# Performance work log

Measured on AMD Instinct MI355X. Metric: run time of the kernel, lower is better.

Reference implementation:

```python
import jax, jax.numpy as jnp
import numpy as np
from jax.scipy.special import gammaln

B, N, F, K = 128, 29, 64, 64
MAXZ, NITER, NPATH = 56, 2, 20
CUTOFF = 5.0


def setup_inputs() -> dict:
    key = jax.random.key(0)
    ks = jax.random.split(key, 16)
    atomic_numbers = jax.random.randint(ks[0], (B, N), 1, MAXZ)
    positions = jax.random.normal(ks[1], (B, N, 3), dtype=jnp.float32) * 2.0
    Ef = jax.random.normal(ks[2], (B, 3), dtype=jnp.float32)
    # fully connected molecular graph (all ordered pairs i != j), E = N*(N-1) = 812
    ii, jj = np.meshgrid(np.arange(N), np.arange(N), indexing="ij")
    m = ii != jj
    dst_idx = jnp.asarray(ii[m], dtype=jnp.int32)
    src_idx = jnp.asarray(jj[m], dtype=jnp.int32)
    s = 1.0 / np.sqrt(F)
    t = 0.2  # tensor-product path weight scale (keeps activations bounded)
    return {
        "atomic_numbers": atomic_numbers, "positions": positions, "Ef": Ef,
        "dst_idx": dst_idx, "src_idx": src_idx,
        "embed": jax.random.normal(ks[3], (MAXZ, F), dtype=jnp.float32) * s,
        "mp_basis_w": jax.random.normal(ks[4], (NITER, K, F), dtype=jnp.float32) / np.sqrt(K),
        "mp_tp_w": jax.random.normal(ks[5], (NITER, NPATH, F), dtype=jnp.float32) * t,
        "d1_w": jax.random.normal(ks[6], (NITER, 2, 2, F, F), dtype=jnp.float32) * s,
        "d1_b": jnp.zeros((NITER, 2, F), dtype=jnp.float32),
        "d2_w": jax.random.normal(ks[7], (NITER, 2, 2, F, F), dtype=jnp.float32) * s,
        "d2_b": jnp.zeros((NITER, 2, F), dtype=jnp.float32),
        "tens_w": jax.random.normal(ks[8], (NITER, NPATH, F), dtype=jnp.float32) * t,
        "td_dense_w": jax.random.normal(ks[9], (NITER, 2, 2, F, F), dtype=jnp.float32) * s,
        "td_tp_w": jax.random.normal(ks[10], (NITER, NPATH, F), dtype=jnp.float32) * t,
        "out_w": jax.random.normal(ks[11], (F,), dtype=jnp.float32) * s,
        "element_bias": jax.random.normal(ks[12], (MAXZ,), dtype=jnp.float32) * 0.1,
    }


def _tp(a, b, w):
    """Channelwise Clebsch-Gordan tensor product for max_degree=1 with parity channels.
    a, b: (M, 2, 4, F) with axis1 = (regular, pseudo), axis2 = (l=0, l=1 x/y/z).
    w: (20, F) learned per-path weights (5 l-paths x 4 parity combos)."""
    M, Fd = a.shape[0], a.shape[-1]
    sr = jnp.zeros((M, Fd), a.dtype); sp = jnp.zeros((M, Fd), a.dtype)
    vr = jnp.zeros((M, 3, Fd), a.dtype); vp = jnp.zeros((M, 3, Fd), a.dtype)
    idx = 0
    for p1 in range(2):
        for p2 in range(2):
            s1 = a[:, p1, 0]; v1 = a[:, p1, 1:4]
            s2 = b[:, p2, 0]; v2 = b[:, p2, 1:4]
            pl0a = 1 - 2 * p1; pl0b = 1 - 2 * p2   # parity of l=0 slot
            pl1a = -(1 - 2 * p1); pl1b = -(1 - 2 * p2)  # parity of l=1 slot
            tt = w[idx] * s1 * s2
            if pl0a * pl0b == 1: sr = sr + tt
            else: sp = sp + tt
            tt = w[idx + 1] * s1[:, None, :] * v2
            if pl0a * pl1b == -1: vr = vr + tt
            else: vp = vp + tt
            tt = w[idx + 2] * v1 * s2[:, None, :]
            if pl1a * pl0b == -1: vr = vr + tt
            else: vp = vp + tt
            tt = w[idx + 3] * jnp.sum(v1 * v2, axis=1)
            if pl1a * pl1b == 1: sr = sr + tt
            else: sp = sp + tt
            tt = w[idx + 4] * jnp.cross(v1, v2, axis=1)
            if pl1a * pl1b == -1: vr = vr + tt
            else: vp = vp + tt
            idx += 5
    reg = jnp.concatenate([sr[:, None, :], vr], axis=1)
    pse = jnp.concatenate([sp[:, None, :], vp], axis=1)
    return jnp.stack([reg, pse], axis=1)  # (M, 2, 4, F)


def _dense(x, W, b=None):
    # per-(parity, degree) linear map over features; W: (2, 2, F, F), b: (2, F)
    s = jnp.einsum("npf,pfg->npg", x[:, :, 0, :], W[:, 0])
    v = jnp.einsum("npdf,pfg->npdg", x[:, :, 1:4, :], W[:, 1])
    if b is not None:
        s = s + b
    return jnp.concatenate([s[:, :, None, :], v], axis=2)


def _silu(x):
    # gated equivariant silu: silu on scalars, sigmoid(scalar) gate on vectors
    s = x[:, :, 0:1, :]
    g = jax.nn.sigmoid(s)
    return jnp.concatenate([s * g, x[:, :, 1:4, :] * g], axis=2)


def _radial(r):
    # reciprocal Bernstein radial basis with smooth cutoff
    k = jnp.arange(K, dtype=r.dtype)
    logc = gammaln(float(K)) - gammaln(k + 1.0) - gammaln(float(K) - k)
    u = 1.0 / (1.0 + r)
    logb = logc + k * jnp.log(u)[:, None] + (K - 1.0 - k) * jnp.log(jnp.maximum(1.0 - u, 1e-12))[:, None]
    x2 = (r / CUTOFF) ** 2
    fcut = jnp.where(x2 < 1.0, jnp.exp(1.0 - 1.0 / jnp.maximum(1.0 - x2, 1e-12)), 0.0)
    return jnp.exp(logb) * fcut[:, None]  # (E, K)


def reference(atomic_numbers, positions, Ef, dst_idx, src_idx, embed, mp_basis_w,
              mp_tp_w, d1_w, d1_b, d2_w, d2_b, tens_w, td_dense_w, td_tp_w,
              out_w, element_bias):
    Bsz, Nn = atomic_numbers.shape
    BN = Bsz * Nn
    Fd = embed.shape[-1]
    pos = positions.reshape(-1, 3)
    Z = atomic_numbers.reshape(-1)
    offsets = (jnp.arange(Bsz, dtype=dst_idx.dtype) * Nn)
    dstf = (dst_idx[None, :] + offsets[:, None]).reshape(-1)  # (B*E,)
    srcf = (src_idx[None, :] + offsets[:, None]).reshape(-1)
    disp = pos[srcf] - pos[dstf]                               # (B*E, 3)
    r = jnp.sqrt(jnp.sum(disp * disp, axis=-1) + 1e-12)
    unit = disp / r[:, None]
    sph = jnp.concatenate([jnp.ones_like(r)[:, None], unit], axis=-1)  # (B*E, 4)
    basis = sph[:, :, None] * _radial(r)[:, None, :]           # (B*E, 4, K)

    x = jnp.zeros((BN, 2, 4, Fd), dtype=positions.dtype)
    x = x.at[:, 0, 0, :].set(embed[Z])

    xEFv = jnp.concatenate([jnp.ones((Bsz, 1), positions.dtype), Ef], axis=-1)  # (B, 4)
    xEF = jnp.repeat(xEFv, Nn, axis=0)                          # (BN, 4)
    xEF = jnp.broadcast_to(xEF[:, None, :, None], (BN, 2, 4, Fd))

    for i in range(NITER):
        bproj = jnp.einsum("edk,kf->edf", basis, mp_basis_w[i])  # (B*E, 4, F)
        bfeat = jnp.stack([bproj, jnp.zeros_like(bproj)], axis=1)  # (B*E, 2, 4, F)
        msg = _tp(x[srcf], bfeat, mp_tp_w[i])
        if i == NITER - 1:  # last iteration: max_degree=0 messages
            msg = msg * jnp.array([1.0, 0.0, 0.0, 0.0], msg.dtype)[None, None, :, None]
        y = jax.ops.segment_sum(msg, dstf, num_segments=BN)
        x = x + y
        h = _dense(x, d1_w[i], d1_b[i])
        h = _silu(h)
        h = _dense(h, d2_w[i], d2_b[i])
        x = h + y
        x = x + _tp(x, xEF, tens_w[i])          # Tensor()(x, xEF)
        x = _tp(x, _dense(x, td_dense_w[i]), td_tp_w[i])  # TensorDense

    s = x[:, 0, 0, :]  # degree-0 regular channel
    atomic_energies = s @ out_w + element_bias[Z]
    energy = atomic_energies.reshape(Bsz, Nn).sum(axis=1)
    return energy
```

## Files before the change

kernel.cpp:

```cpp
#include <hip/hip_runtime.h>

#define NB 128
#define NA 29
#define BN (NB*NA)
#define FD 64


template<bool LAST>
__global__ __launch_bounds__(256) void fmsg_kernel(
    const int*   __restrict__ Z,
    const float* __restrict__ pos,
    const float* __restrict__ src,
    const float* __restrict__ wtp,
    const float* __restrict__ Wb,
    float* __restrict__ y,
    float* __restrict__ out)
{
  __shared__ float elu[28], el1mu[28], efc[28];
  __shared__ float us[28][3];
  __shared__ float rads[28][FD];
  __shared__ float emb_sh[NA][FD];
  __shared__ float yred[4][4][FD];
  const int bn = blockIdx.x, b = bn / NA, n = bn - b*NA;
  const int tid = threadIdx.x, lane = tid & 63, wv = tid >> 6;

  if constexpr (!LAST) {
    if (bn < NB && tid == 0) out[bn] = 0.0f;
  }

  if (tid < 28) {
    const int jr = tid, j = jr + (jr >= n ? 1 : 0);
    const float dx = pos[(b*NA+j)*3+0] - pos[(b*NA+n)*3+0];
    const float dy = pos[(b*NA+j)*3+1] - pos[(b*NA+n)*3+1];
    const float dz = pos[(b*NA+j)*3+2] - pos[(b*NA+n)*3+2];
    const float r  = sqrtf(dx*dx + dy*dy + dz*dz + 1e-12f);
    const float ri = 1.0f / r;
    us[jr][0] = dx*ri; us[jr][1] = dy*ri; us[jr][2] = dz*ri;
    const float u  = 1.0f/(1.0f + r);
    elu[jr]   = logf(u);
    el1mu[jr] = logf(fmaxf(1.0f - u, 1e-12f));
    const float x2 = (r*0.2f)*(r*0.2f);
    efc[jr] = (x2 < 1.0f) ? expf(1.0f - 1.0f/fmaxf(1.0f - x2, 1e-12f)) : 0.0f;
  }
  if constexpr (!LAST) {
    for (int idx = tid; idx < NA*FD; idx += 256)
      emb_sh[idx>>6][idx&63] = src[Z[b*NA + (idx>>6)]*FD + (idx&63)];
  }
  const float kk   = (float)lane;
  const float logc = lgammaf(64.0f) - lgammaf(kk + 1.0f) - lgammaf(64.0f - kk);
  __syncthreads();

  #pragma unroll
  for (int i = 0; i < 7; ++i) {
    const int e = wv*7 + i;
    rads[e][lane] = expf(logc + kk*elu[e] + (63.0f - kk)*el1mu[e]) * efc[e];
  }
  float wb[64];
  #pragma unroll
  for (int k = 0; k < 64; ++k) wb[k] = Wb[k*FD + lane];

  float y0 = 0.0f, y1 = 0.0f, y2 = 0.0f, y3 = 0.0f, y4 = 0.0f;
  const float wm0 = wtp[0*FD + lane];
  const float wm1 = LAST ? 0.0f : wtp[1*FD + lane];
  const float wm3 = LAST ? wtp[3*FD + lane]  : 0.0f;
  const float wm5 = LAST ? wtp[10*FD + lane] : 0.0f;
  const float wm8 = LAST ? wtp[13*FD + lane] : 0.0f;

  #pragma unroll
  for (int i = 0; i < 7; ++i) {
    const int jr = wv*7 + i;
    float a0 = 0.0f;
    #pragma unroll
    for (int k4 = 0; k4 < 16; ++k4) {
      const float4 rv = *(const float4*)&rads[jr][k4*4];
      a0 += wb[k4*4+0]*rv.x + wb[k4*4+1]*rv.y + wb[k4*4+2]*rv.z + wb[k4*4+3]*rv.w;
    }
    const int j = jr + (jr >= n ? 1 : 0);
    const float ux = us[jr][0], uy = us[jr][1], uz = us[jr][2];
    if constexpr (!LAST) {
      const float t0 = a0 * emb_sh[j][lane];
      y0 += wm0*t0;
      const float t1 = wm1*t0;
      y1 += t1*ux; y2 += t1*uy; y3 += t1*uz;
    } else {
      const float* xj = src + (size_t)(b*NA + j)*512 + lane;
      const float s1   = xj[0];
      const float dot1 = xj[64]*ux + xj[128]*uy + xj[192]*uz;
      const float s1p  = xj[256];
      const float dotp = xj[320]*ux + xj[384]*uy + xj[448]*uz;
      y0 += a0*(wm0*s1  + wm3*dot1);
      y4 += a0*(wm5*s1p + wm8*dotp);
    }
  }

  if constexpr (!LAST) {
    yred[wv][0][lane] = y0; yred[wv][1][lane] = y1;
    yred[wv][2][lane] = y2; yred[wv][3][lane] = y3;
  } else {
    yred[wv][0][lane] = y0; yred[wv][1][lane] = y4;
  }
  __syncthreads();
  if (wv == 0) {
    if constexpr (!LAST) {
      #pragma unroll
      for (int c = 0; c < 4; ++c) {
        const float s = yred[0][c][lane] + yred[1][c][lane]
                      + yred[2][c][lane] + yred[3][c][lane];
        y[(size_t)bn*256 + c*64 + lane] = s;
      }
    } else {
      const float s0 = yred[0][0][lane] + yred[1][0][lane]
                     + yred[2][0][lane] + yred[3][0][lane];
      const float s4 = yred[0][1][lane] + yred[1][1][lane]
                     + yred[2][1][lane] + yred[3][1][lane];
      y[(size_t)bn*512 + lane]       = s0;
      y[(size_t)bn*512 + 256 + lane] = s4;
    }
  }
}

__device__ __forceinline__ void tp20(const float* a, const float* bb,
                                     const float* w, float* o)
{
  #pragma unroll
  for (int p1 = 0; p1 < 2; ++p1) {
    #pragma unroll
    for (int p2 = 0; p2 < 2; ++p2) {
      const float* w5 = w + 5*(2*p1 + p2);
      const float s1 = a[p1*4+0], x1 = a[p1*4+1], y1 = a[p1*4+2], z1 = a[p1*4+3];
      const float s2 = bb[p2*4+0], x2 = bb[p2*4+1], y2 = bb[p2*4+2], z2 = bb[p2*4+3];
      const int so = (p1 == p2) ? 0 : 4;
      const int vo = 4 - so;
      o[so+0] += w5[0]*(s1*s2) + w5[3]*(x1*x2 + y1*y2 + z1*z2);
      o[so+1] += w5[1]*(s1*x2) + w5[2]*(x1*s2);
      o[so+2] += w5[1]*(s1*y2) + w5[2]*(y1*s2);
      o[so+3] += w5[1]*(s1*z2) + w5[2]*(z1*s2);
      o[vo+1] += w5[4]*(y1*z2 - z1*y2);
      o[vo+2] += w5[4]*(z1*x2 - x1*z2);
      o[vo+3] += w5[4]*(x1*y2 - y1*x2);
    }
  }
}

__device__ __forceinline__ void stage2(float* __restrict__ wst,
                                       const float* __restrict__ src, int tid)
{
  const float4* s = (const float4*)src;
  float4* d = (float4*)wst;
  #pragma unroll
  for (int i = 0; i < 8; ++i) d[tid + i*256] = s[tid + i*256];
}

__device__ __forceinline__ void denseP2(const float* __restrict__ wst,
                                        const float* __restrict__ rA,
                                        const float* __restrict__ rB,
                                        float bs, int g,
                                        float oA[4], float oB[4])
{
  float a0A = bs, a0B = bs;
  #pragma unroll
  for (int f4 = 0; f4 < 16; ++f4) {
    const float w0 = wst[(f4*4+0)*64+g], w1 = wst[(f4*4+1)*64+g];
    const float w2 = wst[(f4*4+2)*64+g], w3 = wst[(f4*4+3)*64+g];
    const float4 xA = *(const float4*)&rA[f4*4];
    const float4 xB = *(const float4*)&rB[f4*4];
    a0A += w0*xA.x + w1*xA.y + w2*xA.z + w3*xA.w;
    a0B += w0*xB.x + w1*xB.y + w2*xB.z + w3*xB.w;
  }
  oA[0] = a0A; oB[0] = a0B;
  float a1A = 0, a2A = 0, a3A = 0, a1B = 0, a2B = 0, a3B = 0;
  #pragma unroll
  for (int f4 = 0; f4 < 16; ++f4) {
    const float w0 = wst[4096+(f4*4+0)*64+g], w1 = wst[4096+(f4*4+1)*64+g];
    const float w2 = wst[4096+(f4*4+2)*64+g], w3 = wst[4096+(f4*4+3)*64+g];
    const float4 aA = *(const float4*)&rA[ 64+f4*4];
    const float4 bA = *(const float4*)&rA[128+f4*4];
    const float4 cA = *(const float4*)&rA[192+f4*4];
    const float4 aB = *(const float4*)&rB[ 64+f4*4];
    const float4 bB = *(const float4*)&rB[128+f4*4];
    const float4 cB = *(const float4*)&rB[192+f4*4];
    a1A += w0*aA.x + w1*aA.y + w2*aA.z + w3*aA.w;
    a2A += w0*bA.x + w1*bA.y + w2*bA.z + w3*bA.w;
    a3A += w0*cA.x + w1*cA.y + w2*cA.z + w3*cA.w;
    a1B += w0*aB.x + w1*aB.y + w2*aB.z + w3*aB.w;
    a2B += w0*bB.x + w1*bB.y + w2*bB.z + w3*bB.w;
    a3B += w0*cB.x + w1*cB.y + w2*cB.z + w3*cB.w;
  }
  oA[1] = a1A; oA[2] = a2A; oA[3] = a3A;
  oB[1] = a1B; oB[2] = a2B; oB[3] = a3B;
}

template<bool LAST>
__global__ __launch_bounds__(256) void node_kernel(
    const int*   __restrict__ Z,
    const float* __restrict__ embed,
    const float* __restrict__ Ef,
    const float* __restrict__ d1w, const float* __restrict__ d1b,
    const float* __restrict__ d2w, const float* __restrict__ d2b,
    const float* __restrict__ tens_w,
    const float* __restrict__ tdw,
    const float* __restrict__ td_tp_w,
    const float* __restrict__ out_w,
    const float* __restrict__ ebias,
    const float* __restrict__ xin,
    const float* __restrict__ yin,
    float* __restrict__ xout,
    float* __restrict__ out)
{
  __shared__ float wst[2*64*64];
  __shared__ float row[8][8][FD];
  __shared__ float c4_sh[FD];
  const int tid = threadIdx.x, r = tid >> 6, g = tid & 63;
  const int ndA = blockIdx.x*8 + r*2, ndB = ndA + 1;
  float* rowA = &row[r*2+0][0][0];
  float* rowB = &row[r*2+1][0][0];

  if constexpr (!LAST) {
    if (tid < 64) { const float v = d1b[64+tid]; wst[tid] = v/(1.0f + expf(-v)); }
    __syncthreads();
    if (tid < 64) {
      float acc = d2b[64 + tid];
      for (int f = 0; f < 64; ++f) acc += d2w[8192 + f*64 + tid] * wst[f];
      c4_sh[tid] = acc;
    }
    __syncthreads();
  }

  float yA[4], yB[4];
  float y0A = 0, y4A = 0, y0B = 0, y4B = 0;
  if constexpr (!LAST) {
    #pragma unroll
    for (int c = 0; c < 4; ++c) {
      yA[c] = yin[(size_t)ndA*256 + c*64 + g];
      yB[c] = yin[(size_t)ndB*256 + c*64 + g];
    }
    rowA[g] = embed[Z[ndA]*FD + g] + yA[0];
    rowB[g] = embed[Z[ndB]*FD + g] + yB[0];
    #pragma unroll
    for (int c = 1; c < 4; ++c) { rowA[c*64+g] = yA[c]; rowB[c*64+g] = yB[c]; }
  } else {
    y0A = yin[(size_t)ndA*512 + g];     y4A = yin[(size_t)ndA*512 + 256 + g];
    y0B = yin[(size_t)ndB*512 + g];     y4B = yin[(size_t)ndB*512 + 256 + g];
    #pragma unroll
    for (int pc = 0; pc < 8; ++pc) {
      float vA = xin[(size_t)ndA*512 + pc*64 + g];
      float vB = xin[(size_t)ndB*512 + pc*64 + g];
      if (pc == 0) { vA += y0A; vB += y0B; }
      if (pc == 4) { vA += y4A; vB += y4B; }
      rowA[pc*64+g] = vA; rowB[pc*64+g] = vB;
    }
  }
  stage2(wst, d1w, tid);
  __syncthreads();

  {
    float hA[4], hB[4];
    denseP2(wst, rowA, rowB, d1b[g], g, hA, hB);
    const float sA = 1.0f/(1.0f + expf(-hA[0]));
    const float sB = 1.0f/(1.0f + expf(-hB[0]));
    rowA[g] = hA[0]*sA; rowB[g] = hB[0]*sB;
    #pragma unroll
    for (int c = 1; c < 4; ++c) { rowA[c*64+g] = hA[c]*sA; rowB[c*64+g] = hB[c]*sB; }
  }
  __syncthreads();
  if constexpr (LAST) {
    stage2(wst, d1w + 8192, tid);
    __syncthreads();
    float hA[4], hB[4];
    denseP2(wst, rowA + 256, rowB + 256, d1b[64+g], g, hA, hB);
    const float sA = 1.0f/(1.0f + expf(-hA[0]));
    const float sB = 1.0f/(1.0f + expf(-hB[0]));
    rowA[256+g] = hA[0]*sA; rowB[256+g] = hB[0]*sB;
    #pragma unroll
    for (int c = 1; c < 4; ++c) { rowA[256+c*64+g] = hA[c]*sA; rowB[256+c*64+g] = hB[c]*sB; }
    __syncthreads();
  }
  stage2(wst, d2w, tid);
  __syncthreads();

  float x2A[8], x2B[8];
  {
    float oA[4], oB[4];
    denseP2(wst, rowA, rowB, d2b[g], g, oA, oB);
    #pragma unroll
    for (int c = 0; c < 4; ++c) { x2A[c] = oA[c]; x2B[c] = oB[c]; }
  }
  if constexpr (!LAST) {
    #pragma unroll
    for (int c = 0; c < 4; ++c) { x2A[c] += yA[c]; x2B[c] += yB[c]; }
    const float c4v = c4_sh[g];
    x2A[4] = c4v; x2B[4] = c4v;
    x2A[5] = x2A[6] = x2A[7] = 0.0f;
    x2B[5] = x2B[6] = x2B[7] = 0.0f;
  } else {
    x2A[0] += y0A; x2B[0] += y0B;
    __syncthreads();
    stage2(wst, d2w + 8192, tid);
    __syncthreads();
    float oA[4], oB[4];
    denseP2(wst, rowA + 256, rowB + 256, d2b[64+g], g, oA, oB);
    x2A[4] = oA[0] + y4A; x2A[5] = oA[1]; x2A[6] = oA[2]; x2A[7] = oA[3];
    x2B[4] = oB[0] + y4B; x2B[5] = oB[1]; x2B[6] = oB[2]; x2B[7] = oB[3];
  }

  float x3A[8], x3B[8];
  {
    float w20[20];
    #pragma unroll
    for (int q = 0; q < 20; ++q) w20[q] = tens_w[q*FD + g];
    const int bA = ndA / NA, bB = ndB / NA;
    {
      const float bbv[8] = {1.0f, Ef[bA*3+0], Ef[bA*3+1], Ef[bA*3+2],
                            1.0f, Ef[bA*3+0], Ef[bA*3+1], Ef[bA*3+2]};
      float o[8] = {0,0,0,0,0,0,0,0};
      tp20(x2A, bbv, w20, o);
      #pragma unroll
      for (int pc = 0; pc < 8; ++pc) { x3A[pc] = x2A[pc] + o[pc]; rowA[pc*64+g] = x3A[pc]; }
    }
    {
      const float bbv[8] = {1.0f, Ef[bB*3+0], Ef[bB*3+1], Ef[bB*3+2],
                            1.0f, Ef[bB*3+0], Ef[bB*3+1], Ef[bB*3+2]};
      float o[8] = {0,0,0,0,0,0,0,0};
      tp20(x2B, bbv, w20, o);
      #pragma unroll
      for (int pc = 0; pc < 8; ++pc) { x3B[pc] = x2B[pc] + o[pc]; rowB[pc*64+g] = x3B[pc]; }
    }
  }
  __syncthreads();
  stage2(wst, tdw, tid);
  __syncthreads();

  float tdA[8], tdB[8];
  {
    float oA[4], oB[4];
    denseP2(wst, rowA, rowB, 0.0f, g, oA, oB);
    #pragma unroll
    for (int c = 0; c < 4; ++c) { tdA[c] = oA[c]; tdB[c] = oB[c]; }
  }
  __syncthreads();
  stage2(wst, tdw + 8192, tid);
  __syncthreads();
  {
    float oA[4], oB[4];
    denseP2(wst, rowA + 256, rowB + 256, 0.0f, g, oA, oB);
    #pragma unroll
    for (int c = 0; c < 4; ++c) { tdA[4+c] = oA[c]; tdB[4+c] = oB[c]; }
  }

  if constexpr (LAST) {
    const float wa = td_tp_w[0*FD+g],  wb = td_tp_w[3*FD+g];
    const float wc = td_tp_w[15*FD+g], wd = td_tp_w[18*FD+g];
    const float ow = out_w[g];
    float pA = ow * (wa*(x3A[0]*tdA[0])
                   + wb*(x3A[1]*tdA[1] + x3A[2]*tdA[2] + x3A[3]*tdA[3])
                   + wc*(x3A[4]*tdA[4])
                   + wd*(x3A[5]*tdA[5] + x3A[6]*tdA[6] + x3A[7]*tdA[7]));
    float pB = ow * (wa*(x3B[0]*tdB[0])
                   + wb*(x3B[1]*tdB[1] + x3B[2]*tdB[2] + x3B[3]*tdB[3])
                   + wc*(x3B[4]*tdB[4])
                   + wd*(x3B[5]*tdB[5] + x3B[6]*tdB[6] + x3B[7]*tdB[7]));
    #pragma unroll
    for (int off = 32; off > 0; off >>= 1) {
      pA += __shfl_xor(pA, off, 64);
      pB += __shfl_xor(pB, off, 64);
    }
    if (g == 0) {
      atomicAdd(&out[ndA/NA], pA + ebias[Z[ndA]]);
      atomicAdd(&out[ndB/NA], pB + ebias[Z[ndB]]);
    }
  } else {
    float w20[20];
    #pragma unroll
    for (int q = 0; q < 20; ++q) w20[q] = td_tp_w[q*FD + g];
    {
      float o[8] = {0,0,0,0,0,0,0,0};
      tp20(x3A, tdA, w20, o);
      #pragma unroll
      for (int pc = 0; pc < 8; ++pc) xout[(size_t)ndA*512 + pc*64 + g] = o[pc];
    }
    {
      float o[8] = {0,0,0,0,0,0,0,0};
      tp20(x3B, tdB, w20, o);
      #pragma unroll
      for (int pc = 0; pc < 8; ++pc) xout[(size_t)ndB*512 + pc*64 + g] = o[pc];
    }
  }
}

extern "C" void kernel_launch(void* const* d_in, const int* in_sizes, int n_in,
                              void* d_out, int out_size, void* d_ws, size_t ws_size,
                              hipStream_t stream)
{
  (void)in_sizes; (void)n_in; (void)out_size; (void)ws_size;
  const int*   Z     = (const int*)  d_in[0];
  const float* pos   = (const float*)d_in[1];
  const float* Ef    = (const float*)d_in[2];
  const float* embed = (const float*)d_in[5];
  const float* mpbw  = (const float*)d_in[6];
  const float* mptpw = (const float*)d_in[7];
  const float* d1w   = (const float*)d_in[8];
  const float* d1b   = (const float*)d_in[9];
  const float* d2w   = (const float*)d_in[10];
  const float* d2b   = (const float*)d_in[11];
  const float* tensw = (const float*)d_in[12];
  const float* tdw   = (const float*)d_in[13];
  const float* tdtpw = (const float*)d_in[14];
  const float* outw  = (const float*)d_in[15];
  const float* ebias = (const float*)d_in[16];
  float* out = (float*)d_out;

  float* xg = (float*)d_ws;
  float* yg = xg + (size_t)BN*512;

  fmsg_kernel<false><<<BN, 256, 0, stream>>>(Z, pos, embed, mptpw, mpbw, yg, out);
  node_kernel<false><<<BN/8, 256, 0, stream>>>(Z, embed, Ef,
      d1w, d1b, d2w, d2b, tensw, tdw, tdtpw, outw, ebias,
      nullptr, yg, xg, nullptr);
  fmsg_kernel<true><<<BN, 256, 0, stream>>>(Z, pos, xg, mptpw + 1280,
      mpbw + 4096, yg, nullptr);
  node_kernel<true><<<BN/8, 256, 0, stream>>>(Z, embed, Ef,
      d1w + 16384, d1b + 128, d2w + 16384, d2b + 128, tensw + 1280,
      tdw + 16384, tdtpw + 1280, outw, ebias,
      xg, yg, nullptr, out);
}
```

Before: 122.7 us.

## Double-buffer dense weight staging with register prefetch in node kernel

Splits weight staging into a global-to-register load and a register-to-shared write. The next weight matrix is prefetched into registers while the current dense layer computes, and two shared buffers alternate so one barrier per stage replaces two. The c4 constant is now computed by every thread into a register instead of by 64 threads into shared memory, which removes one barrier. In exchange the kernel holds 32 extra registers for the prefetch, and the extra shared buffer may lower occupancy.

```diff
diff --git a/kernel.cpp b/kernel.cpp
--- a/kernel.cpp
+++ b/kernel.cpp
@@ -142,13 +142,19 @@
   }
 }
 
-__device__ __forceinline__ void stage2(float* __restrict__ wst,
-                                       const float* __restrict__ src, int tid)
+__device__ __forceinline__ void stageLoad(float4 L[8],
+                                          const float* __restrict__ src, int tid)
 {
   const float4* s = (const float4*)src;
+  #pragma unroll
+  for (int i = 0; i < 8; ++i) L[i] = s[tid + i*256];
+}
+__device__ __forceinline__ void stageWrite(float* __restrict__ wst,
+                                           const float4 L[8], int tid)
+{
   float4* d = (float4*)wst;
   #pragma unroll
-  for (int i = 0; i < 8; ++i) d[tid + i*256] = s[tid + i*256];
+  for (int i = 0; i < 8; ++i) d[tid + i*256] = L[i];
 }
 
 __device__ __forceinline__ void denseP2(const float* __restrict__ wst,
@@ -207,24 +213,27 @@
     float* __restrict__ xout,
     float* __restrict__ out)
 {
-  __shared__ float wst[2*64*64];
-  __shared__ float row[8][8][FD];
-  __shared__ float c4_sh[FD];
+  __shared__ float wstA[8192];
+  __shared__ float wstB[8192];
+  __shared__ float rows[8][512];
   const int tid = threadIdx.x, r = tid >> 6, g = tid & 63;
   const int ndA = blockIdx.x*8 + r*2, ndB = ndA + 1;
-  float* rowA = &row[r*2+0][0][0];
-  float* rowB = &row[r*2+1][0][0];
-
-  if constexpr (!LAST) {
-    if (tid < 64) { const float v = d1b[64+tid]; wst[tid] = v/(1.0f + expf(-v)); }
-    __syncthreads();
-    if (tid < 64) {
-      float acc = d2b[64 + tid];
-      for (int f = 0; f < 64; ++f) acc += d2w[8192 + f*64 + tid] * wst[f];
-      c4_sh[tid] = acc;
-    }
-    __syncthreads();
-  }
+  float* rowA = rows[r*2+0];
+  float* rowB = rows[r*2+1];
+  float4 L[8];
+
+  float c4r = 0.0f;
+  if constexpr (!LAST) {
+    if (tid < 64) { const float v = d1b[64+tid]; rows[0][tid] = v/(1.0f + expf(-v)); }
+    __syncthreads();
+    float acc = d2b[64 + g];
+    #pragma unroll 8
+    for (int f = 0; f < 64; ++f) acc += d2w[8192 + f*64 + g] * rows[0][f];
+    c4r = acc;
+    __syncthreads();
+  }
+
+  stageLoad(L, d1w, tid);
 
   float yA[4], yB[4];
   float y0A = 0, y4A = 0, y0B = 0, y4B = 0;
@@ -250,61 +259,84 @@
       rowA[pc*64+g] = vA; rowB[pc*64+g] = vB;
     }
   }
-  stage2(wst, d1w, tid);
+  stageWrite(wstA, L, tid);
+  stageLoad(L, LAST ? d1w + 8192 : d2w, tid);
   __syncthreads();
 
   {
     float hA[4], hB[4];
-    denseP2(wst, rowA, rowB, d1b[g], g, hA, hB);
+    denseP2(wstA, rowA, rowB, d1b[g], g, hA, hB);
     const float sA = 1.0f/(1.0f + expf(-hA[0]));
     const float sB = 1.0f/(1.0f + expf(-hB[0]));
     rowA[g] = hA[0]*sA; rowB[g] = hB[0]*sB;
     #pragma unroll
     for (int c = 1; c < 4; ++c) { rowA[c*64+g] = hA[c]*sA; rowB[c*64+g] = hB[c]*sB; }
   }
+  stageWrite(wstB, L, tid);
+  stageLoad(L, LAST ? d2w : tdw, tid);
   __syncthreads();
+
   if constexpr (LAST) {
-    stage2(wst, d1w + 8192, tid);
-    __syncthreads();
     float hA[4], hB[4];
-    denseP2(wst, rowA + 256, rowB + 256, d1b[64+g], g, hA, hB);
+    denseP2(wstB, rowA + 256, rowB + 256, d1b[64+g], g, hA, hB);
     const float sA = 1.0f/(1.0f + expf(-hA[0]));
     const float sB = 1.0f/(1.0f + expf(-hB[0]));
     rowA[256+g] = hA[0]*sA; rowB[256+g] = hB[0]*sB;
     #pragma unroll
     for (int c = 1; c < 4; ++c) { rowA[256+c*64+g] = hA[c]*sA; rowB[256+c*64+g] = hB[c]*sB; }
-    __syncthreads();
-  }
-  stage2(wst, d2w, tid);
-  __syncthreads();
+    stageWrite(wstA, L, tid);
+    stageLoad(L, d2w + 8192, tid);
+    __syncthreads();
+  }
 
   float x2A[8], x2B[8];
   {
     float oA[4], oB[4];
-    denseP2(wst, rowA, rowB, d2b[g], g, oA, oB);
+    denseP2(LAST ? wstA : wstB, rowA, rowB, d2b[g], g, oA, oB);
     #pragma unroll
     for (int c = 0; c < 4; ++c) { x2A[c] = oA[c]; x2B[c] = oB[c]; }
   }
+  float x3A[8], x3B[8];
   if constexpr (!LAST) {
     #pragma unroll
     for (int c = 0; c < 4; ++c) { x2A[c] += yA[c]; x2B[c] += yB[c]; }
-    const float c4v = c4_sh[g];
-    x2A[4] = c4v; x2B[4] = c4v;
+    x2A[4] = c4r; x2B[4] = c4r;
     x2A[5] = x2A[6] = x2A[7] = 0.0f;
     x2B[5] = x2B[6] = x2B[7] = 0.0f;
+    float w20[20];
+    #pragma unroll
+    for (int q = 0; q < 20; ++q) w20[q] = tens_w[q*FD + g];
+    const int bA = ndA / NA, bB = ndB / NA;
+    {
+      const float bbv[8] = {1.0f, Ef[bA*3+0], Ef[bA*3+1], Ef[bA*3+2],
+                            1.0f, Ef[bA*3+0], Ef[bA*3+1], Ef[bA*3+2]};
+      float o[8] = {0,0,0,0,0,0,0,0};
+      tp20(x2A, bbv, w20, o);
+      #pragma unroll
+      for (int pc = 0; pc < 8; ++pc) { x3A[pc] = x2A[pc] + o[pc]; rowA[pc*64+g] = x3A[pc]; }
+    }
+    {
+      const float bbv[8] = {1.0f, Ef[bB*3+0], Ef[bB*3+1], Ef[bB*3+2],
+                            1.0f, Ef[bB*3+0], Ef[bB*3+1], Ef[bB*3+2]};
+      float o[8] = {0,0,0,0,0,0,0,0};
+      tp20(x2B, bbv, w20, o);
+      #pragma unroll
+      for (int pc = 0; pc < 8; ++pc) { x3B[pc] = x2B[pc] + o[pc]; rowB[pc*64+g] = x3B[pc]; }
+    }
+    stageWrite(wstA, L, tid);
+    stageLoad(L, tdw + 8192, tid);
+    __syncthreads();
   } else {
     x2A[0] += y0A; x2B[0] += y0B;
-    __syncthreads();
-    stage2(wst, d2w + 8192, tid);
-    __syncthreads();
-    float oA[4], oB[4];
-    denseP2(wst, rowA + 256, rowB + 256, d2b[64+g], g, oA, oB);
-    x2A[4] = oA[0] + y4A; x2A[5] = oA[1]; x2A[6] = oA[2]; x2A[7] = oA[3];
-    x2B[4] = oB[0] + y4B; x2B[5] = oB[1]; x2B[6] = oB[2]; x2B[7] = oB[3];
-  }
-
-  float x3A[8], x3B[8];
-  {
+    stageWrite(wstB, L, tid);
+    stageLoad(L, tdw, tid);
+    __syncthreads();
+    {
+      float oA[4], oB[4];
+      denseP2(wstB, rowA + 256, rowB + 256, d2b[64+g], g, oA, oB);
+      x2A[4] = oA[0] + y4A; x2A[5] = oA[1]; x2A[6] = oA[2]; x2A[7] = oA[3];
+      x2B[4] = oB[0] + y4B; x2B[5] = oB[1]; x2B[6] = oB[2]; x2B[7] = oB[3];
+    }
     float w20[20];
     #pragma unroll
     for (int q = 0; q < 20; ++q) w20[q] = tens_w[q*FD + g];
@@ -325,24 +357,23 @@
       #pragma unroll
       for (int pc = 0; pc < 8; ++pc) { x3B[pc] = x2B[pc] + o[pc]; rowB[pc*64+g] = x3B[pc]; }
     }
-  }
-  __syncthreads();
-  stage2(wst, tdw, tid);
-  __syncthreads();
+    stageWrite(wstA, L, tid);
+    stageLoad(L, tdw + 8192, tid);
+    __syncthreads();
+  }
 
   float tdA[8], tdB[8];
   {
     float oA[4], oB[4];
-    denseP2(wst, rowA, rowB, 0.0f, g, oA, oB);
+    denseP2(wstA, rowA, rowB, 0.0f, g, oA, oB);
     #pragma unroll
     for (int c = 0; c < 4; ++c) { tdA[c] = oA[c]; tdB[c] = oB[c]; }
   }
-  __syncthreads();
-  stage2(wst, tdw + 8192, tid);
+  stageWrite(wstB, L, tid);
   __syncthreads();
   {
     float oA[4], oB[4];
-    denseP2(wst, rowA + 256, rowB + 256, 0.0f, g, oA, oB);
+    denseP2(wstB, rowA + 256, rowB + 256, 0.0f, g, oA, oB);
     #pragma unroll
     for (int c = 0; c < 4; ++c) { tdA[4+c] = oA[c]; tdB[4+c] = oB[c]; }
   }
```

After: 177.7 us. +44.9%, slower.

## Keep node activations in registers and broadcast via readlane in node dense layers

Applied to the files above, without the earlier changes.

Node-kernel dense layers now keep per-node activations in registers and broadcast each input feature across the wavefront with readlane, instead of staging rows in shared memory. Weights are staged transposed with an XOR swizzle so each lane reads float4 rows of its own output column without bank conflicts. This removes the shared row buffer, the c4 shared buffer and several barriers. The cost is 64 scalar readlanes per input vector per layer plus a more scattered shared-memory store pattern during weight staging.

```diff
diff --git a/kernel.cpp b/kernel.cpp
--- a/kernel.cpp
+++ b/kernel.cpp
@@ -142,49 +142,68 @@
   }
 }
 
-__device__ __forceinline__ void stage2(float* __restrict__ wst,
-                                       const float* __restrict__ src, int tid)
+__device__ __forceinline__ float rl(float v, int l)
+{
+  return __uint_as_float((unsigned)__builtin_amdgcn_readlane((int)__float_as_uint(v), l));
+}
+
+__device__ __forceinline__ void stage2s(float* __restrict__ wst,
+                                        const float* __restrict__ src, int tid)
 {
   const float4* s = (const float4*)src;
   float4* d = (float4*)wst;
   #pragma unroll
-  for (int i = 0; i < 8; ++i) d[tid + i*256] = s[tid + i*256];
-}
-
-__device__ __forceinline__ void denseP2(const float* __restrict__ wst,
-                                        const float* __restrict__ rA,
-                                        const float* __restrict__ rB,
-                                        float bs, int g,
-                                        float oA[4], float oB[4])
-{
+  for (int i = 0; i < 8; ++i) {
+    const int idx = tid + i*256;
+    const int sel = idx >> 10, rem = idx & 1023;
+    const int gg = rem >> 4, f4 = rem & 15;
+    const float4 v = s[idx];
+    const int fline = gg;
+    const int f = rem >> 4;
+    const int g4 = rem & 15;
+    #pragma unroll
+    for (int q = 0; q < 4; ++q) {
+      const int g = g4*4 + q;
+      const int fq = f >> 2, fj = f & 3;
+      ((float*)&d[(sel*64 + g)*16 + (fq ^ (g & 7))])[fj] = (&v.x)[q];
+    }
+    (void)fline;
+  }
+}
+
+__device__ __forceinline__ void denseRL2(
+    const float* __restrict__ wst, int g,
+    float sA, float v1A, float v2A, float v3A,
+    float sB, float v1B, float v2B, float v3B,
+    float bs, float oA[4], float oB[4])
+{
+  const int swb = g & 7;
+  const float4* w0 = (const float4*)wst + g*16;
+  const float4* w1 = (const float4*)wst + (64+g)*16;
   float a0A = bs, a0B = bs;
   #pragma unroll
   for (int f4 = 0; f4 < 16; ++f4) {
-    const float w0 = wst[(f4*4+0)*64+g], w1 = wst[(f4*4+1)*64+g];
-    const float w2 = wst[(f4*4+2)*64+g], w3 = wst[(f4*4+3)*64+g];
-    const float4 xA = *(const float4*)&rA[f4*4];
-    const float4 xB = *(const float4*)&rB[f4*4];
-    a0A += w0*xA.x + w1*xA.y + w2*xA.z + w3*xA.w;
-    a0B += w0*xB.x + w1*xB.y + w2*xB.z + w3*xB.w;
+    const float4 w = w0[f4 ^ swb];
+    #pragma unroll
+    for (int j = 0; j < 4; ++j) {
+      const float wj = (j==0) ? w.x : (j==1) ? w.y : (j==2) ? w.z : w.w;
+      const int f = f4*4 + j;
+      a0A += wj * rl(sA, f);
+      a0B += wj * rl(sB, f);
+    }
   }
   oA[0] = a0A; oB[0] = a0B;
   float a1A = 0, a2A = 0, a3A = 0, a1B = 0, a2B = 0, a3B = 0;
   #pragma unroll
   for (int f4 = 0; f4 < 16; ++f4) {
-    const float w0 = wst[4096+(f4*4+0)*64+g], w1 = wst[4096+(f4*4+1)*64+g];
-    const float w2 = wst[4096+(f4*4+2)*64+g], w3 = wst[4096+(f4*4+3)*64+g];
-    const float4 aA = *(const float4*)&rA[ 64+f4*4];
-    const float4 bA = *(const float4*)&rA[128+f4*4];
-    const float4 cA = *(const float4*)&rA[192+f4*4];
-    const float4 aB = *(const float4*)&rB[ 64+f4*4];
-    const float4 bB = *(const float4*)&rB[128+f4*4];
-    const float4 cB = *(const float4*)&rB[192+f4*4];
-    a1A += w0*aA.x + w1*aA.y + w2*aA.z + w3*aA.w;
-    a2A += w0*bA.x + w1*bA.y + w2*bA.z + w3*bA.w;
-    a3A += w0*cA.x + w1*cA.y + w2*cA.z + w3*cA.w;
-    a1B += w0*aB.x + w1*aB.y + w2*aB.z + w3*aB.w;
-    a2B += w0*bB.x + w1*bB.y + w2*bB.z + w3*bB.w;
-    a3B += w0*cB.x + w1*cB.y + w2*cB.z + w3*cB.w;
+    const float4 w = w1[f4 ^ swb];
+    #pragma unroll
+    for (int j = 0; j < 4; ++j) {
+      const float wj = (j==0) ? w.x : (j==1) ? w.y : (j==2) ? w.z : w.w;
+      const int f = f4*4 + j;
+      a1A += wj * rl(v1A, f); a2A += wj * rl(v2A, f); a3A += wj * rl(v3A, f);
+      a1B += wj * rl(v1B, f); a2B += wj * rl(v2B, f); a3B += wj * rl(v3B, f);
+    }
   }
   oA[1] = a1A; oA[2] = a2A; oA[3] = a3A;
   oB[1] = a1B; oB[2] = a2B; oB[3] = a3B;
@@ -208,24 +227,20 @@
     float* __restrict__ out)
 {
   __shared__ float wst[2*64*64];
-  __shared__ float row[8][8][FD];
-  __shared__ float c4_sh[FD];
   const int tid = threadIdx.x, r = tid >> 6, g = tid & 63;
   const int ndA = blockIdx.x*8 + r*2, ndB = ndA + 1;
-  float* rowA = &row[r*2+0][0][0];
-  float* rowB = &row[r*2+1][0][0];
-
+
+  float c4r = 0.0f;
   if constexpr (!LAST) {
     if (tid < 64) { const float v = d1b[64+tid]; wst[tid] = v/(1.0f + expf(-v)); }
     __syncthreads();
-    if (tid < 64) {
-      float acc = d2b[64 + tid];
-      for (int f = 0; f < 64; ++f) acc += d2w[8192 + f*64 + tid] * wst[f];
-      c4_sh[tid] = acc;
-    }
-    __syncthreads();
-  }
-
+    float acc = d2b[64 + g];
+    #pragma unroll 8
+    for (int f = 0; f < 64; ++f) acc += d2w[8192 + f*64 + g] * wst[f];
+    c4r = acc;
+  }
+
+  float x1A[8], x1B[8];
   float yA[4], yB[4];
   float y0A = 0, y4A = 0, y0B = 0, y4B = 0;
   if constexpr (!LAST) {
@@ -234,10 +249,12 @@
       yA[c] = yin[(size_t)ndA*256 + c*64 + g];
       yB[c] = yin[(size_t)ndB*256 + c*64 + g];
     }
-    rowA[g] = embed[Z[ndA]*FD + g] + yA[0];
-    rowB[g] = embed[Z[ndB]*FD + g] + yB[0];
-    #pragma unroll
-    for (int c = 1; c < 4; ++c) { rowA[c*64+g] = yA[c]; rowB[c*64+g] = yB[c]; }
+    x1A[0] = embed[Z[ndA]*FD + g] + yA[0];
+    x1B[0] = embed[Z[ndB]*FD + g] + yB[0];
+    #pragma unroll
+    for (int c = 1; c < 4; ++c) { x1A[c] = yA[c]; x1B[c] = yB[c]; }
+    #pragma unroll
+    for (int c = 4; c < 8; ++c) { x1A[c] = 0.0f; x1B[c] = 0.0f; }
   } else {
     y0A = yin[(size_t)ndA*512 + g];     y4A = yin[(size_t)ndA*512 + 256 + g];
     y0B = yin[(size_t)ndB*512 + g];     y4B = yin[(size_t)ndB*512 + 256 + g];
@@ -247,58 +264,61 @@
       float vB = xin[(size_t)ndB*512 + pc*64 + g];
       if (pc == 0) { vA += y0A; vB += y0B; }
       if (pc == 4) { vA += y4A; vB += y4B; }
-      rowA[pc*64+g] = vA; rowB[pc*64+g] = vB;
-    }
-  }
-  stage2(wst, d1w, tid);
-  __syncthreads();
-
+      x1A[pc] = vA; x1B[pc] = vB;
+    }
+  }
+
+  __syncthreads();
+  stage2s(wst, d1w, tid);
+  __syncthreads();
+  float hA[4], hB[4];
+  denseRL2(wst, g, x1A[0], x1A[1], x1A[2], x1A[3],
+                   x1B[0], x1B[1], x1B[2], x1B[3], d1b[g], hA, hB);
   {
-    float hA[4], hB[4];
-    denseP2(wst, rowA, rowB, d1b[g], g, hA, hB);
     const float sA = 1.0f/(1.0f + expf(-hA[0]));
     const float sB = 1.0f/(1.0f + expf(-hB[0]));
-    rowA[g] = hA[0]*sA; rowB[g] = hB[0]*sB;
-    #pragma unroll
-    for (int c = 1; c < 4; ++c) { rowA[c*64+g] = hA[c]*sA; rowB[c*64+g] = hB[c]*sB; }
-  }
-  __syncthreads();
+    hA[0] *= sA; hA[1] *= sA; hA[2] *= sA; hA[3] *= sA;
+    hB[0] *= sB; hB[1] *= sB; hB[2] *= sB; hB[3] *= sB;
+  }
+
+  float h2A[4], h2B[4];
   if constexpr (LAST) {
-    stage2(wst, d1w + 8192, tid);
     __syncthreads();
-    float hA[4], hB[4];
-    denseP2(wst, rowA + 256, rowB + 256, d1b[64+g], g, hA, hB);
-    const float sA = 1.0f/(1.0f + expf(-hA[0]));
-    const float sB = 1.0f/(1.0f + expf(-hB[0]));
-    rowA[256+g] = hA[0]*sA; rowB[256+g] = hB[0]*sB;
-    #pragma unroll
-    for (int c = 1; c < 4; ++c) { rowA[256+c*64+g] = hA[c]*sA; rowB[256+c*64+g] = hB[c]*sB; }
+    stage2s(wst, d1w + 8192, tid);
     __syncthreads();
-  }
-  stage2(wst, d2w, tid);
-  __syncthreads();
-
+    denseRL2(wst, g, x1A[4], x1A[5], x1A[6], x1A[7],
+                     x1B[4], x1B[5], x1B[6], x1B[7], d1b[64+g], h2A, h2B);
+    const float sA = 1.0f/(1.0f + expf(-h2A[0]));
+    const float sB = 1.0f/(1.0f + expf(-h2B[0]));
+    h2A[0] *= sA; h2A[1] *= sA; h2A[2] *= sA; h2A[3] *= sA;
+    h2B[0] *= sB; h2B[1] *= sB; h2B[2] *= sB; h2B[3] *= sB;
+  }
+
+  __syncthreads();
+  stage2s(wst, d2w, tid);
+  __syncthreads();
   float x2A[8], x2B[8];
   {
     float oA[4], oB[4];
-    denseP2(wst, rowA, rowB, d2b[g], g, oA, oB);
+    denseRL2(wst, g, hA[0], hA[1], hA[2], hA[3],
+                     hB[0], hB[1], hB[2], hB[3], d2b[g], oA, oB);
     #pragma unroll
     for (int c = 0; c < 4; ++c) { x2A[c] = oA[c]; x2B[c] = oB[c]; }
   }
   if constexpr (!LAST) {
     #pragma unroll
     for (int c = 0; c < 4; ++c) { x2A[c] += yA[c]; x2B[c] += yB[c]; }
-    const float c4v = c4_sh[g];
-    x2A[4] = c4v; x2B[4] = c4v;
+    x2A[4] = c4r; x2B[4] = c4r;
     x2A[5] = x2A[6] = x2A[7] = 0.0f;
     x2B[5] = x2B[6] = x2B[7] = 0.0f;
   } else {
     x2A[0] += y0A; x2B[0] += y0B;
     __syncthreads();
-    stage2(wst, d2w + 8192, tid);
+    stage2s(wst, d2w + 8192, tid);
     __syncthreads();
     float oA[4], oB[4];
-    denseP2(wst, rowA + 256, rowB + 256, d2b[64+g], g, oA, oB);
+    denseRL2(wst, g, h2A[0], h2A[1], h2A[2], h2A[3],
+                     h2B[0], h2B[1], h2B[2], h2B[3], d2b[64+g], oA, oB);
     x2A[4] = oA[0] + y4A; x2A[5] = oA[1]; x2A[6] = oA[2]; x2A[7] = oA[3];
     x2B[4] = oB[0] + y4B; x2B[5] = oB[1]; x2B[6] = oB[2]; x2B[7] = oB[3];
   }
@@ -315,7 +335,7 @@
       float o[8] = {0,0,0,0,0,0,0,0};
       tp20(x2A, bbv, w20, o);
       #pragma unroll
-      for (int pc = 0; pc < 8; ++pc) { x3A[pc] = x2A[pc] + o[pc]; rowA[pc*64+g] = x3A[pc]; }
+      for (int pc = 0; pc < 8; ++pc) x3A[pc] = x2A[pc] + o[pc];
     }
     {
       const float bbv[8] = {1.0f, Ef[bB*3+0], Ef[bB*3+1], Ef[bB*3+2],
@@ -323,26 +343,28 @@
       float o[8] = {0,0,0,0,0,0,0,0};
       tp20(x2B, bbv, w20, o);
       #pragma unroll
-      for (int pc = 0; pc < 8; ++pc) { x3B[pc] = x2B[pc] + o[pc]; rowB[pc*64+g] = x3B[pc]; }
-    }
-  }
-  __syncthreads();
-  stage2(wst, tdw, tid);
-  __syncthreads();
-
+      for (int pc = 0; pc < 8; ++pc) x3B[pc] = x2B[pc] + o[pc];
+    }
+  }
+
+  __syncthreads();
+  stage2s(wst, tdw, tid);
+  __syncthreads();
   float tdA[8], tdB[8];
   {
     float oA[4], oB[4];
-    denseP2(wst, rowA, rowB, 0.0f, g, oA, oB);
+    denseRL2(wst, g, x3A[0], x3A[1], x3A[2], x3A[3],
+                     x3B[0], x3B[1], x3B[2], x3B[3], 0.0f, oA, oB);
     #pragma unroll
     for (int c = 0; c < 4; ++c) { tdA[c] = oA[c]; tdB[c] = oB[c]; }
   }
   __syncthreads();
-  stage2(wst, tdw + 8192, tid);
+  stage2s(wst, tdw + 8192, tid);
   __syncthreads();
   {
     float oA[4], oB[4];
-    denseP2(wst, rowA + 256, rowB + 256, 0.0f, g, oA, oB);
+    denseRL2(wst, g, x3A[4], x3A[5], x3A[6], x3A[7],
+                     x3B[4], x3B[5], x3B[6], x3B[7], 0.0f, oA, oB);
     #pragma unroll
     for (int c = 0; c < 4; ++c) { tdA[4+c] = oA[c]; tdB[4+c] = oB[c]; }
   }
```

Measured after the change: 142.9 us. +16.5%, slower.
